# Kernel tuning notes

Hardware: AMD Instinct MI355X
Metric: run time of the kernel (lower is better)

Reference implementation:

```python
import jax, jax.numpy as jnp
import numpy as np
from jax import lax

B, N, S = 16, 8192, 512
BASE_K = 16
MS_K = (8, 16, 24)


def _fps(xyz, npoint):
    # farthest point sampling; xyz [B,N,3] -> indices [B,npoint]
    b, n, _ = xyz.shape
    def body(carry, _):
        dists, far = carry
        c = jnp.take_along_axis(xyz, far[:, None, None], axis=1)  # [B,1,3]
        d = jnp.sum((xyz - c) ** 2, -1)
        dists = jnp.minimum(dists, d)
        return (dists, jnp.argmax(dists, -1).astype(jnp.int32)), far
    init = (jnp.full((b, n), 1e10, xyz.dtype), jnp.zeros((b,), jnp.int32))
    _, idx = lax.scan(body, init, None, length=npoint)
    return idx.swapaxes(0, 1)  # [B,npoint]


def _sqdist(a, b):
    # a [B,S,3], b [B,N,3] -> squared distances [B,S,N] (same topk order as cdist)
    return (jnp.sum(a * a, -1)[:, :, None] + jnp.sum(b * b, -1)[:, None, :]
            - 2.0 * jnp.einsum('bsc,bnc->bsn', a, b))


def _gather(pts, idx):
    # pts [B,N,C], idx [B,S,K] -> [B,S,K,C]
    b = pts.shape[0]
    return pts[jnp.arange(b)[:, None, None], idx]


def setup_inputs():
    key = jax.random.key(0)
    ks = jax.random.split(key, 6)
    s = 0.05
    return {
        'l0_xyz': jax.random.normal(ks[0], (B, 3, N), jnp.float32),
        'l0_points': jax.random.normal(ks[1], (B, 3, N), jnp.float32),
        'sa_W1': jax.random.normal(ks[2], (64, 6), jnp.float32) * s,
        'sa_b1': jnp.zeros((64,), jnp.float32),
        'sa_W2': jax.random.normal(ks[3], (128, 64), jnp.float32) * s,
        'sa_b2': jnp.zeros((128,), jnp.float32),
        'ms_W1': jax.random.normal(ks[4], (3, 64, 3), jnp.float32) * s,
        'ms_b1': jnp.zeros((3, 64), jnp.float32),
        'ms_W2': jax.random.normal(ks[5], (3, 128, 64), jnp.float32) * s,
        'ms_b2': jnp.zeros((3, 128), jnp.float32),
    }


def reference(l0_xyz, l0_points, sa_W1, sa_b1, sa_W2, sa_b2, ms_W1, ms_b1, ms_W2, ms_b2):
    xyz = l0_xyz.swapaxes(1, 2)     # [B,N,3]
    pts = l0_points.swapaxes(1, 2)  # [B,N,3]
    # --- PointNet_SA_Module_KNN: FPS + KNN grouping + shared MLP + max-pool ---
    fps_idx = _fps(lax.stop_gradient(xyz), S)                         # [B,S]
    new_xyz = jnp.take_along_axis(xyz, fps_idx[:, :, None], axis=1)  # [B,S,3]
    d = _sqdist(lax.stop_gradient(new_xyz), lax.stop_gradient(xyz))  # [B,S,N]
    _, knn_idx = lax.top_k(-d, BASE_K)                                # [B,S,K]
    g_xyz = _gather(xyz, knn_idx) - new_xyz[:, :, None]               # [B,S,K,3]
    g_pts = _gather(pts, knn_idx)                                     # [B,S,K,3]
    feat = jnp.concatenate([g_xyz, g_pts], -1)                        # [B,S,K,6]
    h = jax.nn.relu(jnp.einsum('bskc,oc->bsko', feat, sa_W1) + sa_b1)
    h = jnp.einsum('bsko,po->bskp', h, sa_W2) + sa_b2
    base_feat = jnp.max(h, axis=2)                                    # [B,S,128]
    keypoints = new_xyz.swapaxes(1, 2)                                # [B,3,S]
    # --- multi-scale: no_grad cdist, per-scale topk + rel-coord MLP + max-pool ---
    dist = _sqdist(lax.stop_gradient(new_xyz), lax.stop_gradient(xyz))  # [B,S,N]
    feats = [base_feat.swapaxes(1, 2)]                                  # [B,128,S]
    for i, k in enumerate(MS_K):
        k_eff = min(k, N)
        _, idx = lax.top_k(-dist, k_eff)                                # [B,S,k]
        rel = _gather(xyz, idx) - new_xyz[:, :, None]                   # [B,S,k,3]
        h = jax.nn.relu(jnp.einsum('bskc,oc->bsko', rel, ms_W1[i]) + ms_b1[i])
        h = jnp.einsum('bsko,po->bskp', h, ms_W2[i]) + ms_b2[i]
        feats.append(jnp.max(h, axis=2).swapaxes(1, 2))                 # [B,128,S]
    return keypoints, jnp.concatenate(feats, axis=1)                    # [B,3,S],[B,512,S]
```

## Files before the change

kernel.cpp:

```cpp
#include <hip/hip_runtime.h>

#define BB 16
#define NN 8192
#define SS 512
#define N3 (3 * NN)
#define KD 14

typedef unsigned short u16;
typedef unsigned int u32;
typedef unsigned long long u64;
typedef float v2f __attribute__((ext_vector_type(2)));

__device__ __forceinline__ v2f pk_add(v2f a, v2f b) {
  v2f r;
  asm("v_pk_add_f32 %0, %1, %2" : "=v"(r) : "v"(a), "v"(b));
  return r;
}
__device__ __forceinline__ v2f pk_mul(v2f a, v2f b) {
  v2f r;
  asm("v_pk_mul_f32 %0, %1, %2" : "=v"(r) : "v"(a), "v"(b));
  return r;
}

template <int CTRL>
__device__ __forceinline__ float dpp_maxf(float x) {
  int m = __builtin_amdgcn_update_dpp(0, __float_as_int(x), CTRL, 0xf, 0xf, false);
  return fmaxf(x, __int_as_float(m));
}
template <int CTRL>
__device__ __forceinline__ u32 dpp_maxu(u32 x) {
  u32 m = (u32)__builtin_amdgcn_update_dpp(0, (int)x, CTRL, 0xf, 0xf, false);
  return (x > m) ? x : m;
}

__global__ __attribute__((amdgpu_flat_work_group_size(256, 256),
                          amdgpu_waves_per_eu(1, 1)))
void k_fps(const float* __restrict__ xyz, float* __restrict__ out_kp) {
  __shared__ int sIdx[SS];
  __shared__ float sv[4];
  __shared__ u32 si[4];
  int b = blockIdx.x, t = threadIdx.x;
  const float* base = xyz + b * N3;
  v2f px[16], py[16], pz[16], dm[16];
#pragma unroll
  for (int j = 0; j < 16; ++j) {
    int n0 = j * 512 + t, n1 = n0 + 256;
    px[j] = v2f{base[n0], base[n1]};
    py[j] = v2f{base[NN + n0], base[NN + n1]};
    pz[j] = v2f{base[2 * NN + n0], base[2 * NN + n1]};
    dm[j] = v2f{1e10f, 1e10f};
  }
#pragma unroll
  for (int j = 0; j < 16; ++j) {
    asm volatile("" : "+v"(px[j]), "+v"(py[j]), "+v"(pz[j]));
  }
  float cx = base[0], cy = base[NN], cz = base[2 * NN];
  int far = 0;
  int lane = t & 63, w = t >> 6;
  u32 tb = (u32)(NN - t);
  for (int it = 0; it < SS; ++it) {
    if (t == 0) sIdx[it] = far;
    v2f ncx = v2f{-cx, -cx}, ncy = v2f{-cy, -cy}, ncz = v2f{-cz, -cz};
    float vmax = 0.0f;
#pragma unroll
    for (int j = 0; j < 16; ++j) {
      v2f dx = pk_add(px[j], ncx);
      v2f dy = pk_add(py[j], ncy);
      v2f dz = pk_add(pz[j], ncz);
      v2f xx = pk_mul(dx, dx);
      v2f yy = pk_mul(dy, dy);
      v2f s = pk_add(xx, yy);
      v2f zz = pk_mul(dz, dz);
      v2f d = pk_add(s, zz);
      float a0 = fminf(dm[j].x, d.x);
      float a1 = fminf(dm[j].y, d.y);
      dm[j].x = a0;
      dm[j].y = a1;
      vmax = fmaxf(vmax, a0);
      vmax = fmaxf(vmax, a1);
    }
    vmax = dpp_maxf<0x111>(vmax);
    vmax = dpp_maxf<0x112>(vmax);
    vmax = dpp_maxf<0x114>(vmax);
    vmax = dpp_maxf<0x118>(vmax);
    vmax = dpp_maxf<0x142>(vmax);
    vmax = dpp_maxf<0x143>(vmax);
    if (lane == 63) sv[w] = vmax;
    __syncthreads();
    float vg = fmaxf(fmaxf(sv[0], sv[1]), fmaxf(sv[2], sv[3]));
    u32 cand = 0;
#pragma unroll
    for (int j = 15; j >= 0; --j) {
      u32 v1 = tb - (u32)(j * 512 + 256);
      u32 v0 = tb - (u32)(j * 512);
      cand = (dm[j].y == vg) ? v1 : cand;
      cand = (dm[j].x == vg) ? v0 : cand;
    }
    cand = dpp_maxu<0x111>(cand);
    cand = dpp_maxu<0x112>(cand);
    cand = dpp_maxu<0x114>(cand);
    cand = dpp_maxu<0x118>(cand);
    cand = dpp_maxu<0x142>(cand);
    cand = dpp_maxu<0x143>(cand);
    if (lane == 63) si[w] = cand;
    __syncthreads();
    u32 c01 = (si[0] > si[1]) ? si[0] : si[1];
    u32 c23 = (si[2] > si[3]) ? si[2] : si[3];
    u32 cg = (c01 > c23) ? c01 : c23;
    far = NN - (int)cg;
    cx = base[far];
    cy = base[NN + far];
    cz = base[2 * NN + far];
  }
  __syncthreads();
  for (int i = t; i < SS; i += 256) {
    int id = sIdx[i];
    out_kp[b * 1536 + i] = base[id];
    out_kp[b * 1536 + SS + i] = base[NN + id];
    out_kp[b * 1536 + 2 * SS + i] = base[2 * NN + id];
  }
}

__global__ __launch_bounds__(256) void k_knn(const float* __restrict__ xyz,
                                             const float* __restrict__ kp,
                                             u16* __restrict__ knn) {
  int t = threadIdx.x;
  int row = blockIdx.x * 4 + (t >> 6);
  int lane = t & 63;
  int b = row >> 9, s = row & (SS - 1);
  const float* base = xyz + b * N3;
  float ax = kp[b * 1536 + s];
  float ay = kp[b * 1536 + SS + s];
  float az = kp[b * 1536 + 2 * SS + s];
  float aw = __fadd_rn(__fadd_rn(__fmul_rn(ax, ax), __fmul_rn(ay, ay)), __fmul_rn(az, az));
  u64 arr[KD];
#pragma unroll
  for (int i = 0; i < KD; ++i) arr[i] = ~0ull;
  for (int c = 0; c < 128; ++c) {
    int n = c * 64 + lane;
    float qx = base[n], qy = base[NN + n], qz = base[2 * NN + n];
    float qw = __fadd_rn(__fadd_rn(__fmul_rn(qx, qx), __fmul_rn(qy, qy)), __fmul_rn(qz, qz));
    float dot = __fadd_rn(__fadd_rn(__fmul_rn(ax, qx), __fmul_rn(ay, qy)), __fmul_rn(az, qz));
    float d = __fsub_rn(__fadd_rn(aw, qw), __fmul_rn(2.0f, dot));
    u32 ub = __float_as_uint(d);
    ub ^= (ub & 0x80000000u) ? 0xFFFFFFFFu : 0x80000000u;
    u64 key = ((u64)ub << 32) | (u32)n;
    if (key < arr[KD - 1]) {
#pragma unroll
      for (int i = KD - 1; i >= 1; --i) {
        u64 am = arr[i - 1];
        arr[i] = (am > key) ? am : ((arr[i] > key) ? key : arr[i]);
      }
      if (arr[0] > key) arr[0] = key;
    }
  }
  u64 mine = 0;
  for (int it = 0; it < 24; ++it) {
    u64 m = arr[0];
#pragma unroll
    for (int off = 1; off < 64; off <<= 1) {
      u64 o = __shfl_xor(m, off, 64);
      m = (o < m) ? o : m;
    }
    if (lane == it) mine = m;
    if (arr[0] == m) {
#pragma unroll
      for (int i = 0; i < KD - 1; ++i) arr[i] = arr[i + 1];
      arr[KD - 1] = ~0ull;
    }
  }
  if (lane < 24) knn[row * 24 + lane] = (u16)(mine & 0xFFFFu);
}

__global__ __launch_bounds__(256) void k_base(
    const float* __restrict__ xyz, const float* __restrict__ pts,
    const float* __restrict__ kp, const u16* __restrict__ knn,
    const float* __restrict__ W1, const float* __restrict__ b1,
    const float* __restrict__ W2, const float* __restrict__ b2,
    float* __restrict__ out) {
  __shared__ float sW1T[6 * 64];
  __shared__ float sb1[64];
  __shared__ float sfeat[4][16 * 6];
  __shared__ float sh1[4][16 * 64];
  int t = threadIdx.x, lane = t & 63, w = t >> 6;
  int b = blockIdx.x >> 6, s0 = (blockIdx.x & 63) * 8;
  for (int i = t; i < 384; i += 256) {
    int o = i / 6, c = i - o * 6;
    sW1T[c * 64 + o] = W1[i];
  }
  if (t < 64) sb1[t] = b1[t];
  float wgtA[64], wgtB[64];
#pragma unroll
  for (int j = 0; j < 64; ++j) {
    wgtA[j] = W2[lane * 64 + j];
    wgtB[j] = W2[(lane + 64) * 64 + j];
  }
  float b2A = b2[lane], b2B = b2[lane + 64];
  __syncthreads();
  for (int g = 0; g < 2; ++g) {
    for (int i = t; i < 384; i += 256) {
      int rr = i / 96, rem = i - rr * 96, k = rem / 6, c = rem - k * 6;
      int s = s0 + g * 4 + rr, row = b * SS + s;
      int id = knn[row * 24 + k];
      float val;
      if (c < 3) {
        val = __fsub_rn(xyz[b * N3 + c * NN + id], kp[b * 1536 + c * SS + s]);
      } else {
        val = pts[b * N3 + (c - 3) * NN + id];
      }
      sfeat[rr][k * 6 + c] = val;
    }
    __syncthreads();
#pragma unroll
    for (int m = 0; m < 16; ++m) {
      int u = m * 256 + t;
      int rr = u >> 10, rem = u & 1023, k = rem >> 6, o = rem & 63;
      float acc = sb1[o];
#pragma unroll
      for (int c = 0; c < 6; ++c) acc = fmaf(sfeat[rr][k * 6 + c], sW1T[c * 64 + o], acc);
      sh1[rr][k * 64 + o] = fmaxf(acc, 0.f);
    }
    __syncthreads();
    float bestA = -1e30f, bestB = -1e30f;
#pragma unroll
    for (int k = 0; k < 16; ++k) {
      const float4* h4 = (const float4*)&sh1[w][k * 64];
      float a0 = 0.f, a1 = 0.f;
#pragma unroll
      for (int j = 0; j < 16; ++j) {
        float4 hv = h4[j];
        a0 = fmaf(hv.x, wgtA[4 * j], a0);
        a0 = fmaf(hv.y, wgtA[4 * j + 1], a0);
        a0 = fmaf(hv.z, wgtA[4 * j + 2], a0);
        a0 = fmaf(hv.w, wgtA[4 * j + 3], a0);
        a1 = fmaf(hv.x, wgtB[4 * j], a1);
        a1 = fmaf(hv.y, wgtB[4 * j + 1], a1);
        a1 = fmaf(hv.z, wgtB[4 * j + 2], a1);
        a1 = fmaf(hv.w, wgtB[4 * j + 3], a1);
      }
      bestA = fmaxf(bestA, a0);
      bestB = fmaxf(bestB, a1);
    }
    int s = s0 + g * 4 + w;
    out[24576 + b * 262144 + lane * 512 + s] = bestA + b2A;
    out[24576 + b * 262144 + (lane + 64) * 512 + s] = bestB + b2B;
    __syncthreads();
  }
}

__global__ __launch_bounds__(256) void k_ms(
    const float* __restrict__ xyz, const float* __restrict__ kp,
    const u16* __restrict__ knn, const float* __restrict__ msW1,
    const float* __restrict__ msb1, const float* __restrict__ msW2,
    const float* __restrict__ msb2, float* __restrict__ out) {
  int scale = blockIdx.y;
  int kk = 8 * (scale + 1);
  __shared__ float sW1T[3 * 64];
  __shared__ float sb1[64];
  __shared__ float sfeat[4][24 * 3];
  __shared__ float sh1[4][24 * 64];
  int t = threadIdx.x, lane = t & 63, w = t >> 6;
  int b = blockIdx.x >> 6, s0 = (blockIdx.x & 63) * 8;
  const float* W1s = msW1 + scale * 192;
  for (int i = t; i < 192; i += 256) {
    int o = i / 3, c = i - o * 3;
    sW1T[c * 64 + o] = W1s[i];
  }
  if (t < 64) sb1[t] = msb1[scale * 64 + t];
  float wgtA[64], wgtB[64];
#pragma unroll
  for (int j = 0; j < 64; ++j) {
    wgtA[j] = msW2[scale * 8192 + lane * 64 + j];
    wgtB[j] = msW2[scale * 8192 + (lane + 64) * 64 + j];
  }
  float b2A = msb2[scale * 128 + lane], b2B = msb2[scale * 128 + lane + 64];
  __syncthreads();
  int co = 128 * (scale + 1);
  for (int g = 0; g < 2; ++g) {
    int nfeat = 4 * kk * 3;
    for (int i = t; i < nfeat; i += 256) {
      int kk3 = kk * 3;
      int rr = i / kk3, rem = i - rr * kk3, k = rem / 3, c = rem - k * 3;
      int s = s0 + g * 4 + rr, row = b * SS + s;
      int id = knn[row * 24 + k];
      sfeat[rr][k * 3 + c] = __fsub_rn(xyz[b * N3 + c * NN + id], kp[b * 1536 + c * SS + s]);
    }
    __syncthreads();
    for (int rr = 0; rr < 4; ++rr) {
      for (int u = t; u < kk * 64; u += 256) {
        int k = u >> 6, o = u & 63;
        float acc = sb1[o];
        acc = fmaf(sfeat[rr][k * 3 + 0], sW1T[o], acc);
        acc = fmaf(sfeat[rr][k * 3 + 1], sW1T[64 + o], acc);
        acc = fmaf(sfeat[rr][k * 3 + 2], sW1T[128 + o], acc);
        sh1[rr][k * 64 + o] = fmaxf(acc, 0.f);
      }
    }
    __syncthreads();
    float bestA = -1e30f, bestB = -1e30f;
    for (int k = 0; k < kk; ++k) {
      const float4* h4 = (const float4*)&sh1[w][k * 64];
      float a0 = 0.f, a1 = 0.f;
#pragma unroll
      for (int j = 0; j < 16; ++j) {
        float4 hv = h4[j];
        a0 = fmaf(hv.x, wgtA[4 * j], a0);
        a0 = fmaf(hv.y, wgtA[4 * j + 1], a0);
        a0 = fmaf(hv.z, wgtA[4 * j + 2], a0);
        a0 = fmaf(hv.w, wgtA[4 * j + 3], a0);
        a1 = fmaf(hv.x, wgtB[4 * j], a1);
        a1 = fmaf(hv.y, wgtB[4 * j + 1], a1);
        a1 = fmaf(hv.z, wgtB[4 * j + 2], a1);
        a1 = fmaf(hv.w, wgtB[4 * j + 3], a1);
      }
      bestA = fmaxf(bestA, a0);
      bestB = fmaxf(bestB, a1);
    }
    int s = s0 + g * 4 + w;
    out[24576 + b * 262144 + (co + lane) * 512 + s] = bestA + b2A;
    out[24576 + b * 262144 + (co + lane + 64) * 512 + s] = bestB + b2B;
    __syncthreads();
  }
}

extern "C" void kernel_launch(void* const* d_in, const int* in_sizes, int n_in,
                              void* d_out, int out_size, void* d_ws, size_t ws_size,
                              hipStream_t stream) {
  const float* xyz = (const float*)d_in[0];
  const float* pts = (const float*)d_in[1];
  const float* sa_W1 = (const float*)d_in[2];
  const float* sa_b1 = (const float*)d_in[3];
  const float* sa_W2 = (const float*)d_in[4];
  const float* sa_b2 = (const float*)d_in[5];
  const float* ms_W1 = (const float*)d_in[6];
  const float* ms_b1 = (const float*)d_in[7];
  const float* ms_W2 = (const float*)d_in[8];
  const float* ms_b2 = (const float*)d_in[9];
  float* out = (float*)d_out;
  const float* kp = (const float*)d_out;

  u16* knn = (u16*)d_ws;

  k_fps<<<BB, 256, 0, stream>>>(xyz, out);
  k_knn<<<(BB * SS) / 4, 256, 0, stream>>>(xyz, kp, knn);
  k_base<<<BB * 64, 256, 0, stream>>>(xyz, pts, kp, knn, sa_W1, sa_b1, sa_W2, sa_b2, out);
  k_ms<<<dim3(BB * 64, 3), 256, 0, stream>>>(xyz, kp, knn, ms_W1, ms_b1, ms_W2, ms_b2, out);
}
```

Baseline: 1.087 ms.

## Cut FPS to one barrier per iteration with packed value-index keys and LDS coords

The farthest-point-sampling loop now reduces each wave's max distance and winning index together as a packed 64-bit key, so each iteration needs a single block barrier instead of two. A double-buffered shared slot avoids a write-after-read race without adding a second barrier. Point coordinates are also staged in LDS (96KB), so the next centroid is read from shared memory instead of global memory on the serial critical path. The trade-off is large LDS use and a costlier 64-bit compare; per-wave index selection now uses the wave's own max.

```diff
diff --git a/kernel.cpp b/kernel.cpp
--- a/kernel.cpp
+++ b/kernel.cpp
@@ -36,9 +36,9 @@
 __global__ __attribute__((amdgpu_flat_work_group_size(256, 256),
                           amdgpu_waves_per_eu(1, 1)))
 void k_fps(const float* __restrict__ xyz, float* __restrict__ out_kp) {
+  __shared__ float sxyz[NN * 3];
   __shared__ int sIdx[SS];
-  __shared__ float sv[4];
-  __shared__ u32 si[4];
+  __shared__ u64 rkey[2][4];
   int b = blockIdx.x, t = threadIdx.x;
   const float* base = xyz + b * N3;
   v2f px[16], py[16], pz[16], dm[16];
@@ -49,6 +49,12 @@
     py[j] = v2f{base[NN + n0], base[NN + n1]};
     pz[j] = v2f{base[2 * NN + n0], base[2 * NN + n1]};
     dm[j] = v2f{1e10f, 1e10f};
+    sxyz[n0 * 3 + 0] = px[j].x;
+    sxyz[n0 * 3 + 1] = py[j].x;
+    sxyz[n0 * 3 + 2] = pz[j].x;
+    sxyz[n1 * 3 + 0] = px[j].y;
+    sxyz[n1 * 3 + 1] = py[j].y;
+    sxyz[n1 * 3 + 2] = pz[j].y;
   }
 #pragma unroll
   for (int j = 0; j < 16; ++j) {
@@ -76,8 +82,7 @@
       float a1 = fminf(dm[j].y, d.y);
       dm[j].x = a0;
       dm[j].y = a1;
-      vmax = fmaxf(vmax, a0);
-      vmax = fmaxf(vmax, a1);
+      vmax = fmaxf(vmax, fmaxf(a0, a1));
     }
     vmax = dpp_maxf<0x111>(vmax);
     vmax = dpp_maxf<0x112>(vmax);
@@ -85,16 +90,14 @@
     vmax = dpp_maxf<0x118>(vmax);
     vmax = dpp_maxf<0x142>(vmax);
     vmax = dpp_maxf<0x143>(vmax);
-    if (lane == 63) sv[w] = vmax;
-    __syncthreads();
-    float vg = fmaxf(fmaxf(sv[0], sv[1]), fmaxf(sv[2], sv[3]));
+    float wv = __int_as_float(__builtin_amdgcn_readlane(__float_as_int(vmax), 63));
     u32 cand = 0;
 #pragma unroll
     for (int j = 15; j >= 0; --j) {
       u32 v1 = tb - (u32)(j * 512 + 256);
       u32 v0 = tb - (u32)(j * 512);
-      cand = (dm[j].y == vg) ? v1 : cand;
-      cand = (dm[j].x == vg) ? v0 : cand;
+      cand = (dm[j].y == wv) ? v1 : cand;
+      cand = (dm[j].x == wv) ? v0 : cand;
     }
     cand = dpp_maxu<0x111>(cand);
     cand = dpp_maxu<0x112>(cand);
@@ -102,15 +105,18 @@
     cand = dpp_maxu<0x118>(cand);
     cand = dpp_maxu<0x142>(cand);
     cand = dpp_maxu<0x143>(cand);
-    if (lane == 63) si[w] = cand;
-    __syncthreads();
-    u32 c01 = (si[0] > si[1]) ? si[0] : si[1];
-    u32 c23 = (si[2] > si[3]) ? si[2] : si[3];
-    u32 cg = (c01 > c23) ? c01 : c23;
-    far = NN - (int)cg;
-    cx = base[far];
-    cy = base[NN + far];
-    cz = base[2 * NN + far];
+    int pb = it & 1;
+    if (lane == 63) rkey[pb][w] = ((u64)__float_as_uint(wv) << 32) | cand;
+    __syncthreads();
+    u64 k0 = rkey[pb][0], k1 = rkey[pb][1];
+    u64 k2 = rkey[pb][2], k3 = rkey[pb][3];
+    u64 k01 = (k0 > k1) ? k0 : k1;
+    u64 k23 = (k2 > k3) ? k2 : k3;
+    u64 kg = (k01 > k23) ? k01 : k23;
+    far = NN - (int)(u32)(kg & 0xffffffffu);
+    cx = sxyz[far * 3 + 0];
+    cy = sxyz[far * 3 + 1];
+    cz = sxyz[far * 3 + 2];
   }
   __syncthreads();
   for (int i = t; i < SS; i += 256) {
```

Measured after the change: 1.031 ms. 5.2% less time.
